# Optimization experiments

Hardware: AMD Instinct MI355X
Metric: run time of the kernel (lower is better)

The kernel has to match this reference:

```python
import jax, jax.numpy as jnp
import numpy as np

B, H, W, C = 32, 64, 64, 256


def setup_inputs() -> dict:
    key = jax.random.key(0)
    kq, kk, kv = jax.random.split(key, 3)
    query = jax.random.normal(kq, (B, H, W, C), dtype=jnp.float32)
    keys = jax.random.normal(kk, (B, H, W, C), dtype=jnp.float32)
    values = jax.random.normal(kv, (B, H, W, C), dtype=jnp.float32)
    return {"query": query, "keys": keys, "values": values}


def reference(query, keys, values):
    # A[b,q,k] = sum_{h,w} query[b,h,w,q] * keys[b,h,w,k]
    scores = jnp.einsum("bhwq,bhwk->bqk", query, keys)
    attn = jax.nn.softmax(scores, axis=-1)  # softmax over keys axis
    # out[b,q,h,w] = sum_k attn[b,q,k] * values[b,h,w,k]
    out = jnp.einsum("bqk,bhwk->bqhw", attn, values)
    return out
```

## Files before the change

kernel.cpp:

```cpp
#include <hip/hip_runtime.h>
#include <hip/hip_bf16.h>

#define B_  32
#define HW_ 4096
#define C_  256
#define S_LDS 40

using bf16x8 = __attribute__((ext_vector_type(8))) short;
using f32x4  = __attribute__((ext_vector_type(4))) float;
using u32x4  = __attribute__((ext_vector_type(4))) uint;

__device__ __forceinline__ ushort f2bf_rn(float x) {
    uint u = __builtin_bit_cast(uint, x);
    u += 0x7FFFu + ((u >> 16) & 1u);
    return (ushort)(u >> 16);
}
__device__ __forceinline__ uint pk_bf2(float a, float b) {
    return ((uint)f2bf_rn(b) << 16) | (uint)f2bf_rn(a);
}
__device__ __forceinline__ uint pk_rtz(float x0, float x1) {
    return __builtin_amdgcn_perm(__builtin_bit_cast(uint, x1),
                                 __builtin_bit_cast(uint, x0), 0x07060302u);
}
__device__ __forceinline__ void split2_rtz(float x0, float x1, uint& hi2, uint& lo2) {
    uint u0 = __builtin_bit_cast(uint, x0), u1 = __builtin_bit_cast(uint, x1);
    hi2 = __builtin_amdgcn_perm(u1, u0, 0x07060302u);
    float h0 = __builtin_bit_cast(float, u0 & 0xFFFF0000u);
    float h1 = __builtin_bit_cast(float, u1 & 0xFFFF0000u);
    lo2 = pk_rtz(x0 - h0, x1 - h1);
}

__global__ __launch_bounds__(256, 4) void scores_kernel(const float* __restrict__ qg,
                                                        const float* __restrict__ kg,
                                                        float* __restrict__ dst,
                                                        long slabStride) {
    int x  = blockIdx.x;
    int s  = x & 3;
    int tn = (x >> 2) & 3;
    int tm = (x >> 4) & 1;
    int b  = x >> 5;

    __shared__ __align__(16) ushort Qhi[128 * S_LDS], Qlo[128 * S_LDS];
    __shared__ __align__(16) ushort Khi[64 * S_LDS],  Klo[64 * S_LDS];

    int tid = threadIdx.x, lane = tid & 63, w = tid >> 6;
    int m0 = (w >> 1) * 64;
    int n0 = (w & 1) * 32;
    int g = lane >> 4, r16 = lane & 15;

    int cq = tid & 127;
    int hq = (tid >> 7) * 16;
    int ck = tid & 63;
    int hk = (tid >> 6) * 8;

    const float* qcol = qg + (size_t)b * HW_ * C_ + tm * 128 + cq;
    const float* kcol = kg + (size_t)b * HW_ * C_ + tn * 64 + ck;

    f32x4 acc[4][2];
#pragma unroll
    for (int i = 0; i < 4; ++i)
#pragma unroll
        for (int j = 0; j < 2; ++j) acc[i][j] = (f32x4){0.f, 0.f, 0.f, 0.f};

#define LOAD_QK(qr, kr, itv) {                                                 \
        int hw0 = s * 1024 + (itv) * 32;                                       \
        const float* qp = qcol + (size_t)(hw0 + hq) * C_;                      \
        _Pragma("unroll")                                                      \
        for (int j = 0; j < 16; ++j) qr[j] = qp[(size_t)j * C_];               \
        const float* kp = kcol + (size_t)(hw0 + hk) * C_;                      \
        _Pragma("unroll")                                                      \
        for (int j = 0; j < 8; ++j) kr[j] = kp[(size_t)j * C_];                \
    }

#define CONVERT_STORE(qr, kr) {                                                \
        uint qh[8], ql[8];                                                     \
        _Pragma("unroll")                                                      \
        for (int p = 0; p < 8; ++p) split2_rtz(qr[2*p], qr[2*p+1], qh[p], ql[p]); \
        int qb_ = cq * S_LDS + hq;                                             \
        *reinterpret_cast<u32x4*>(&Qhi[qb_])     = (u32x4){qh[0], qh[1], qh[2], qh[3]}; \
        *reinterpret_cast<u32x4*>(&Qhi[qb_ + 8]) = (u32x4){qh[4], qh[5], qh[6], qh[7]}; \
        *reinterpret_cast<u32x4*>(&Qlo[qb_])     = (u32x4){ql[0], ql[1], ql[2], ql[3]}; \
        *reinterpret_cast<u32x4*>(&Qlo[qb_ + 8]) = (u32x4){ql[4], ql[5], ql[6], ql[7]}; \
        uint kh[4], kl[4];                                                     \
        _Pragma("unroll")                                                      \
        for (int p = 0; p < 4; ++p) split2_rtz(kr[2*p], kr[2*p+1], kh[p], kl[p]); \
        int kb_ = ck * S_LDS + hk;                                             \
        *reinterpret_cast<u32x4*>(&Khi[kb_]) = (u32x4){kh[0], kh[1], kh[2], kh[3]}; \
        *reinterpret_cast<u32x4*>(&Klo[kb_]) = (u32x4){kl[0], kl[1], kl[2], kl[3]}; \
    }

#define MFMA_PHASE() {                                                         \
        __builtin_amdgcn_s_setprio(1);                                         \
        bf16x8 ahi[4], alo[4];                                                 \
        _Pragma("unroll")                                                      \
        for (int mi = 0; mi < 4; ++mi) {                                       \
            int off = (m0 + mi * 16 + r16) * S_LDS + g * 8;                    \
            ahi[mi] = *reinterpret_cast<const bf16x8*>(&Qhi[off]);             \
            alo[mi] = *reinterpret_cast<const bf16x8*>(&Qlo[off]);             \
        }                                                                      \
        _Pragma("unroll")                                                      \
        for (int ni = 0; ni < 2; ++ni) {                                       \
            int off = (n0 + ni * 16 + r16) * S_LDS + g * 8;                    \
            bf16x8 bhi = *reinterpret_cast<const bf16x8*>(&Khi[off]);          \
            bf16x8 blo = *reinterpret_cast<const bf16x8*>(&Klo[off]);          \
            _Pragma("unroll")                                                  \
            for (int mi = 0; mi < 4; ++mi) {                                   \
                acc[mi][ni] = __builtin_amdgcn_mfma_f32_16x16x32_bf16(ahi[mi], bhi, acc[mi][ni], 0, 0, 0); \
                acc[mi][ni] = __builtin_amdgcn_mfma_f32_16x16x32_bf16(ahi[mi], blo, acc[mi][ni], 0, 0, 0); \
                acc[mi][ni] = __builtin_amdgcn_mfma_f32_16x16x32_bf16(alo[mi], bhi, acc[mi][ni], 0, 0, 0); \
            }                                                                  \
        }                                                                      \
        __builtin_amdgcn_s_setprio(0);                                         \
    }

#define STEP(qc, kc, qn, kn, itv, doload) {                                    \
        if (doload) LOAD_QK(qn, kn, (itv) + 1);                                \
        __syncthreads();                                                       \
        CONVERT_STORE(qc, kc);                                                 \
        __syncthreads();                                                       \
        MFMA_PHASE();                                                          \
    }

    float qa[16], ka[8], qb[16], kb[8];
    LOAD_QK(qa, ka, 0);
    for (int p = 0; p < 16; ++p) {
        STEP(qa, ka, qb, kb, 2 * p, true);
        STEP(qb, kb, qa, ka, 2 * p + 1, p < 15);
    }

    float* base = dst + (size_t)s * slabStride;
#pragma unroll
    for (int mi = 0; mi < 4; ++mi)
#pragma unroll
        for (int ni = 0; ni < 2; ++ni)
#pragma unroll
            for (int r = 0; r < 4; ++r) {
                int qrow = tm * 128 + m0 + mi * 16 + g * 4 + r;
                int kc   = tn * 64 + n0 + ni * 16 + r16;
                float* p = base + ((size_t)b * 256 + qrow) * 256 + kc;
                if (slabStride) *p = acc[mi][ni][r];
                else            atomicAdd(p, acc[mi][ni][r]);
            }
#undef STEP
#undef MFMA_PHASE
#undef CONVERT_STORE
#undef LOAD_QK
}

__global__ __launch_bounds__(256) void softmax_kernel(const float* __restrict__ scores,
                                                      ushort* __restrict__ attn,
                                                      int nslab, long slabStride) {
    int wid  = blockIdx.x * 4 + (threadIdx.x >> 6);
    int lane = threadIdx.x & 63;
    const float* p0 = scores + (size_t)wid * 256 + lane * 4;
    float4 v = *reinterpret_cast<const float4*>(p0);
    for (int sl = 1; sl < nslab; ++sl) {
        const float4 t = *reinterpret_cast<const float4*>(p0 + (size_t)sl * slabStride);
        v.x += t.x; v.y += t.y; v.z += t.z; v.w += t.w;
    }
    float m = fmaxf(fmaxf(v.x, v.y), fmaxf(v.z, v.w));
#pragma unroll
    for (int off = 32; off; off >>= 1) m = fmaxf(m, __shfl_xor(m, off, 64));
    float e0 = __expf(v.x - m), e1 = __expf(v.y - m), e2 = __expf(v.z - m), e3 = __expf(v.w - m);
    float ssum = e0 + e1 + e2 + e3;
#pragma unroll
    for (int off = 32; off; off >>= 1) ssum += __shfl_xor(ssum, off, 64);
    float inv = 1.0f / ssum;
    uint2 o;
    o.x = pk_bf2(e0 * inv, e1 * inv);
    o.y = pk_bf2(e2 * inv, e3 * inv);
    *reinterpret_cast<uint2*>(attn + (size_t)wid * 256 + lane * 4) = o;
}

__global__ __launch_bounds__(256, 4) void pv_kernel(const ushort* __restrict__ attn,
                                                    const float* __restrict__ vg,
                                                    float* __restrict__ out) {
    int b   = blockIdx.x >> 6;
    int hw0 = (blockIdx.x & 63) * 64;
    int tid = threadIdx.x, lane = tid & 63, w = tid >> 6;
    int m0  = w * 64;
    int g   = lane >> 4, r16 = lane & 15;

    __shared__ __align__(16) float Vt[2 * 64 * 32];

    int srow = tid >> 2;
    int sslot = (tid & 3) * 2;
    int wi0 = srow * 32 + ((sslot ^ (srow & 7)) * 4);
    int wi1 = srow * 32 + (((sslot + 1) ^ (srow & 7)) * 4);
    const float* vstage = vg + ((size_t)(b * HW_ + hw0 + srow)) * C_ + sslot * 4;

    const ushort* abase = attn + (size_t)b * 256 * 256 + g * 8;

    f32x4 acc[4][4];
#pragma unroll
    for (int i = 0; i < 4; ++i)
#pragma unroll
        for (int j = 0; j < 4; ++j) acc[i][j] = (f32x4){0.f, 0.f, 0.f, 0.f};

    {
        f32x4 p0 = *reinterpret_cast<const f32x4*>(vstage);
        f32x4 p1 = *reinterpret_cast<const f32x4*>(vstage + 4);
        *reinterpret_cast<f32x4*>(&Vt[wi0]) = p0;
        *reinterpret_cast<f32x4*>(&Vt[wi1]) = p1;
    }
    __syncthreads();

    for (int p = 0; p < 8; ++p) {
        float* rbuf = &Vt[(p & 1) * 64 * 32];
        float* wbuf = &Vt[((p + 1) & 1) * 64 * 32];

        f32x4 n0v, n1v;
        if (p < 7) {
            n0v = *reinterpret_cast<const f32x4*>(vstage + (p + 1) * 32);
            n1v = *reinterpret_cast<const f32x4*>(vstage + (p + 1) * 32 + 4);
        }

        int k0 = p * 32;
        bf16x8 a[4];
#pragma unroll
        for (int mi = 0; mi < 4; ++mi)
            a[mi] = *reinterpret_cast<const bf16x8*>(abase + (size_t)(m0 + mi * 16 + r16) * 256 + k0);

#pragma unroll
        for (int ni = 0; ni < 4; ++ni) {
            int row = ni * 16 + r16, key = row & 7;
            f32x4 f0 = *reinterpret_cast<const f32x4*>(&rbuf[row * 32 + (((2 * g)     ^ key) * 4)]);
            f32x4 f1 = *reinterpret_cast<const f32x4*>(&rbuf[row * 32 + (((2 * g + 1) ^ key) * 4)]);
            bf16x8 bf = __builtin_bit_cast(bf16x8, (u32x4){
                pk_rtz(f0[0], f0[1]), pk_rtz(f0[2], f0[3]),
                pk_rtz(f1[0], f1[1]), pk_rtz(f1[2], f1[3])});
#pragma unroll
            for (int mi = 0; mi < 4; ++mi)
                acc[mi][ni] = __builtin_amdgcn_mfma_f32_16x16x32_bf16(a[mi], bf, acc[mi][ni], 0, 0, 0);
        }

        if (p < 7) {
            *reinterpret_cast<f32x4*>(&wbuf[wi0]) = n0v;
            *reinterpret_cast<f32x4*>(&wbuf[wi1]) = n1v;
            __syncthreads();
        }
    }

#pragma unroll
    for (int mi = 0; mi < 4; ++mi)
#pragma unroll
        for (int ni = 0; ni < 4; ++ni)
#pragma unroll
            for (int r = 0; r < 4; ++r) {
                int qrow = m0 + mi * 16 + g * 4 + r;
                int hw   = hw0 + ni * 16 + r16;
                out[((size_t)b * 256 + qrow) * 4096 + hw] = acc[mi][ni][r];
            }
}

extern "C" void kernel_launch(void* const* d_in, const int* in_sizes, int n_in,
                              void* d_out, int out_size, void* d_ws, size_t ws_size,
                              hipStream_t stream) {
    const float* q = (const float*)d_in[0];
    const float* k = (const float*)d_in[1];
    const float* v = (const float*)d_in[2];
    float* out = (float*)d_out;

    const size_t slab = (size_t)B_ * 256 * 256;
    const size_t needBytes = 4 * slab * 4 + slab * 2;
    float* scores = (float*)d_ws;

    if (ws_size >= needBytes) {
        ushort* attn = (ushort*)((char*)d_ws + 4 * slab * 4);
        scores_kernel<<<1024, 256, 0, stream>>>(q, k, scores, (long)slab);
        softmax_kernel<<<2048, 256, 0, stream>>>(scores, attn, 4, (long)slab);
        pv_kernel<<<2048, 256, 0, stream>>>(attn, v, out);
    } else {
        ushort* attn = (ushort*)((char*)d_ws + slab * 4);
        (void)hipMemsetAsync(d_ws, 0, slab * 4, stream);
        scores_kernel<<<1024, 256, 0, stream>>>(q, k, scores, 0L);
        softmax_kernel<<<2048, 256, 0, stream>>>(scores, attn, 1, 0L);
        pv_kernel<<<2048, 256, 0, stream>>>(attn, v, out);
    }
}
```

Baseline: 176.2 us.

## Load float2 pairs, triple-buffer global prefetch, and reorder block-index decomposition

The scores kernel now loads two adjacent channels per thread as float2 instead of scalar floats, which halves the number of load instructions. It also keeps three register buffers so global loads are issued two iterations ahead instead of one. The block index decomposition now puts tn and tm in the low bits so neighbouring blocks share the same HW slab, which may improve L2 locality. Occupancy hint is lowered from 4 to 3 blocks per CU to make room for the extra prefetch registers, at the cost of fewer resident waves.

After: 202.7 us. 15.1% more time.

```diff
diff --git a/kernel.cpp b/kernel.cpp
--- a/kernel.cpp
+++ b/kernel.cpp
@@ -30,14 +30,14 @@
     lo2 = pk_rtz(x0 - h0, x1 - h1);
 }
 
-__global__ __launch_bounds__(256, 4) void scores_kernel(const float* __restrict__ qg,
+__global__ __launch_bounds__(256, 3) void scores_kernel(const float* __restrict__ qg,
                                                         const float* __restrict__ kg,
                                                         float* __restrict__ dst,
                                                         long slabStride) {
     int x  = blockIdx.x;
-    int s  = x & 3;
-    int tn = (x >> 2) & 3;
-    int tm = (x >> 4) & 1;
+    int tn = x & 3;
+    int tm = (x >> 2) & 1;
+    int s  = (x >> 3) & 3;
     int b  = x >> 5;
 
     __shared__ __align__(16) ushort Qhi[128 * S_LDS], Qlo[128 * S_LDS];
@@ -48,13 +48,13 @@
     int n0 = (w & 1) * 32;
     int g = lane >> 4, r16 = lane & 15;
 
-    int cq = tid & 127;
-    int hq = (tid >> 7) * 16;
-    int ck = tid & 63;
-    int hk = (tid >> 6) * 8;
-
-    const float* qcol = qg + (size_t)b * HW_ * C_ + tm * 128 + cq;
-    const float* kcol = kg + (size_t)b * HW_ * C_ + tn * 64 + ck;
+    int qpair = tid & 63;
+    int hb    = (tid >> 6) * 8;
+    int kpair = tid & 31;
+    int hk    = (tid >> 5) * 4;
+
+    const float2* qbase2 = (const float2*)qg + (size_t)b * HW_ * 128 + tm * 64 + qpair;
+    const float2* kbase2 = (const float2*)kg + (size_t)b * HW_ * 128 + tn * 32 + kpair;
 
     f32x4 acc[4][2];
 #pragma unroll
@@ -62,31 +62,43 @@
 #pragma unroll
         for (int j = 0; j < 2; ++j) acc[i][j] = (f32x4){0.f, 0.f, 0.f, 0.f};
 
-#define LOAD_QK(qr, kr, itv) {                                                 \
+#define LOADQK(qr, kr, itv) {                                                  \
         int hw0 = s * 1024 + (itv) * 32;                                       \
-        const float* qp = qcol + (size_t)(hw0 + hq) * C_;                      \
-        _Pragma("unroll")                                                      \
-        for (int j = 0; j < 16; ++j) qr[j] = qp[(size_t)j * C_];               \
-        const float* kp = kcol + (size_t)(hw0 + hk) * C_;                      \
-        _Pragma("unroll")                                                      \
-        for (int j = 0; j < 8; ++j) kr[j] = kp[(size_t)j * C_];                \
+        const float2* qp = qbase2 + (size_t)(hw0 + hb) * 128;                  \
+        _Pragma("unroll")                                                      \
+        for (int j = 0; j < 8; ++j) qr[j] = qp[(size_t)j * 128];               \
+        const float2* kp = kbase2 + (size_t)(hw0 + hk) * 128;                  \
+        _Pragma("unroll")                                                      \
+        for (int j = 0; j < 4; ++j) kr[j] = kp[(size_t)j * 128];               \
     }
 
 #define CONVERT_STORE(qr, kr) {                                                \
-        uint qh[8], ql[8];                                                     \
-        _Pragma("unroll")                                                      \
-        for (int p = 0; p < 8; ++p) split2_rtz(qr[2*p], qr[2*p+1], qh[p], ql[p]); \
-        int qb_ = cq * S_LDS + hq;                                             \
-        *reinterpret_cast<u32x4*>(&Qhi[qb_])     = (u32x4){qh[0], qh[1], qh[2], qh[3]}; \
-        *reinterpret_cast<u32x4*>(&Qhi[qb_ + 8]) = (u32x4){qh[4], qh[5], qh[6], qh[7]}; \
-        *reinterpret_cast<u32x4*>(&Qlo[qb_])     = (u32x4){ql[0], ql[1], ql[2], ql[3]}; \
-        *reinterpret_cast<u32x4*>(&Qlo[qb_ + 8]) = (u32x4){ql[4], ql[5], ql[6], ql[7]}; \
-        uint kh[4], kl[4];                                                     \
-        _Pragma("unroll")                                                      \
-        for (int p = 0; p < 4; ++p) split2_rtz(kr[2*p], kr[2*p+1], kh[p], kl[p]); \
-        int kb_ = ck * S_LDS + hk;                                             \
-        *reinterpret_cast<u32x4*>(&Khi[kb_]) = (u32x4){kh[0], kh[1], kh[2], kh[3]}; \
-        *reinterpret_cast<u32x4*>(&Klo[kb_]) = (u32x4){kl[0], kl[1], kl[2], kl[3]}; \
+        uint h_[4], l_[4];                                                     \
+        split2_rtz(qr[0].x, qr[1].x, h_[0], l_[0]);                            \
+        split2_rtz(qr[2].x, qr[3].x, h_[1], l_[1]);                            \
+        split2_rtz(qr[4].x, qr[5].x, h_[2], l_[2]);                            \
+        split2_rtz(qr[6].x, qr[7].x, h_[3], l_[3]);                            \
+        int r0 = (2 * qpair) * S_LDS + hb;                                     \
+        *reinterpret_cast<u32x4*>(&Qhi[r0]) = (u32x4){h_[0], h_[1], h_[2], h_[3]}; \
+        *reinterpret_cast<u32x4*>(&Qlo[r0]) = (u32x4){l_[0], l_[1], l_[2], l_[3]}; \
+        split2_rtz(qr[0].y, qr[1].y, h_[0], l_[0]);                            \
+        split2_rtz(qr[2].y, qr[3].y, h_[1], l_[1]);                            \
+        split2_rtz(qr[4].y, qr[5].y, h_[2], l_[2]);                            \
+        split2_rtz(qr[6].y, qr[7].y, h_[3], l_[3]);                            \
+        int r1 = (2 * qpair + 1) * S_LDS + hb;                                 \
+        *reinterpret_cast<u32x4*>(&Qhi[r1]) = (u32x4){h_[0], h_[1], h_[2], h_[3]}; \
+        *reinterpret_cast<u32x4*>(&Qlo[r1]) = (u32x4){l_[0], l_[1], l_[2], l_[3]}; \
+        uint ha, hb2, la, lb;                                                  \
+        split2_rtz(kr[0].x, kr[1].x, ha, la);                                  \
+        split2_rtz(kr[2].x, kr[3].x, hb2, lb);                                 \
+        int rk0 = (2 * kpair) * S_LDS + hk;                                    \
+        *reinterpret_cast<uint2*>(&Khi[rk0]) = make_uint2(ha, hb2);            \
+        *reinterpret_cast<uint2*>(&Klo[rk0]) = make_uint2(la, lb);             \
+        split2_rtz(kr[0].y, kr[1].y, ha, la);                                  \
+        split2_rtz(kr[2].y, kr[3].y, hb2, lb);                                 \
+        int rk1 = (2 * kpair + 1) * S_LDS + hk;                                \
+        *reinterpret_cast<uint2*>(&Khi[rk1]) = make_uint2(ha, hb2);            \
+        *reinterpret_cast<uint2*>(&Klo[rk1]) = make_uint2(la, lb);             \
     }
 
 #define MFMA_PHASE() {                                                         \
@@ -114,19 +126,23 @@
     }
 
 #define STEP(qc, kc, qn, kn, itv, doload) {                                    \
-        if (doload) LOAD_QK(qn, kn, (itv) + 1);                                \
+        if (doload) LOADQK(qn, kn, (itv) + 2);                                 \
         __syncthreads();                                                       \
         CONVERT_STORE(qc, kc);                                                 \
         __syncthreads();                                                       \
         MFMA_PHASE();                                                          \
     }
 
-    float qa[16], ka[8], qb[16], kb[8];
-    LOAD_QK(qa, ka, 0);
-    for (int p = 0; p < 16; ++p) {
-        STEP(qa, ka, qb, kb, 2 * p, true);
-        STEP(qb, kb, qa, ka, 2 * p + 1, p < 15);
-    }
+    float2 qA[8], qB[8], qC[8], kA[4], kB[4], kC[4];
+    LOADQK(qA, kA, 0);
+    LOADQK(qB, kB, 1);
+    for (int p = 0; p < 10; ++p) {
+        STEP(qA, kA, qC, kC, 3 * p,     true);
+        STEP(qB, kB, qA, kA, 3 * p + 1, true);
+        STEP(qC, kC, qB, kB, 3 * p + 2, true);
+    }
+    STEP(qA, kA, qC, kC, 30, false);
+    STEP(qB, kB, qC, kC, 31, false);
 
     float* base = dst + (size_t)s * slabStride;
 #pragma unroll
@@ -144,7 +160,7 @@
 #undef STEP
 #undef MFMA_PHASE
 #undef CONVERT_STORE
-#undef LOAD_QK
+#undef LOADQK
 }
 
 __global__ __launch_bounds__(256) void softmax_kernel(const float* __restrict__ scores,
```

## Enlarge scores tile to 128x128 with 8-way split-K over HW

Applied to the files above, without the earlier changes.

The scores GEMM tile grows from 128x64 to 128x128 per block, so each loaded Q element is reused across twice as many key columns. This reduces redundant global reads of Q. To keep the same block count, split-K over the spatial axis doubles from 4 to 8 slabs, which doubles the partial-score workspace and the number of slabs the softmax kernel must sum. The larger accumulator raises register pressure, so the launch-bounds occupancy hint drops from 4 to 3 blocks.

Result: slower. 193.5 us (+9.8%).

```diff
diff --git a/kernel.cpp b/kernel.cpp
--- a/kernel.cpp
+++ b/kernel.cpp
@@ -30,63 +30,61 @@
     lo2 = pk_rtz(x0 - h0, x1 - h1);
 }
 
-__global__ __launch_bounds__(256, 4) void scores_kernel(const float* __restrict__ qg,
+__global__ __launch_bounds__(256, 3) void scores_kernel(const float* __restrict__ qg,
                                                         const float* __restrict__ kg,
                                                         float* __restrict__ dst,
                                                         long slabStride) {
     int x  = blockIdx.x;
-    int s  = x & 3;
-    int tn = (x >> 2) & 3;
+    int s  = x & 7;
+    int tn = (x >> 3) & 1;
     int tm = (x >> 4) & 1;
     int b  = x >> 5;
 
     __shared__ __align__(16) ushort Qhi[128 * S_LDS], Qlo[128 * S_LDS];
-    __shared__ __align__(16) ushort Khi[64 * S_LDS],  Klo[64 * S_LDS];
+    __shared__ __align__(16) ushort Khi[128 * S_LDS], Klo[128 * S_LDS];
 
     int tid = threadIdx.x, lane = tid & 63, w = tid >> 6;
     int m0 = (w >> 1) * 64;
-    int n0 = (w & 1) * 32;
+    int n0 = (w & 1) * 64;
     int g = lane >> 4, r16 = lane & 15;
 
-    int cq = tid & 127;
-    int hq = (tid >> 7) * 16;
-    int ck = tid & 63;
-    int hk = (tid >> 6) * 8;
-
-    const float* qcol = qg + (size_t)b * HW_ * C_ + tm * 128 + cq;
-    const float* kcol = kg + (size_t)b * HW_ * C_ + tn * 64 + ck;
-
-    f32x4 acc[4][2];
+    int cc = tid & 127;
+    int hh = (tid >> 7) * 16;
+
+    const float* qcol = qg + (size_t)b * HW_ * C_ + tm * 128 + cc;
+    const float* kcol = kg + (size_t)b * HW_ * C_ + tn * 128 + cc;
+
+    f32x4 acc[4][4];
 #pragma unroll
     for (int i = 0; i < 4; ++i)
 #pragma unroll
-        for (int j = 0; j < 2; ++j) acc[i][j] = (f32x4){0.f, 0.f, 0.f, 0.f};
+        for (int j = 0; j < 4; ++j) acc[i][j] = (f32x4){0.f, 0.f, 0.f, 0.f};
 
 #define LOAD_QK(qr, kr, itv) {                                                 \
-        int hw0 = s * 1024 + (itv) * 32;                                       \
-        const float* qp = qcol + (size_t)(hw0 + hq) * C_;                      \
+        int hw0 = s * 512 + (itv) * 32 + hh;                                   \
+        const float* qp = qcol + (size_t)hw0 * C_;                             \
+        const float* kp = kcol + (size_t)hw0 * C_;                             \
         _Pragma("unroll")                                                      \
         for (int j = 0; j < 16; ++j) qr[j] = qp[(size_t)j * C_];               \
-        const float* kp = kcol + (size_t)(hw0 + hk) * C_;                      \
-        _Pragma("unroll")                                                      \
-        for (int j = 0; j < 8; ++j) kr[j] = kp[(size_t)j * C_];                \
+        _Pragma("unroll")                                                      \
+        for (int j = 0; j < 16; ++j) kr[j] = kp[(size_t)j * C_];               \
     }
 
 #define CONVERT_STORE(qr, kr) {                                                \
-        uint qh[8], ql[8];                                                     \
-        _Pragma("unroll")                                                      \
-        for (int p = 0; p < 8; ++p) split2_rtz(qr[2*p], qr[2*p+1], qh[p], ql[p]); \
-        int qb_ = cq * S_LDS + hq;                                             \
-        *reinterpret_cast<u32x4*>(&Qhi[qb_])     = (u32x4){qh[0], qh[1], qh[2], qh[3]}; \
-        *reinterpret_cast<u32x4*>(&Qhi[qb_ + 8]) = (u32x4){qh[4], qh[5], qh[6], qh[7]}; \
-        *reinterpret_cast<u32x4*>(&Qlo[qb_])     = (u32x4){ql[0], ql[1], ql[2], ql[3]}; \
-        *reinterpret_cast<u32x4*>(&Qlo[qb_ + 8]) = (u32x4){ql[4], ql[5], ql[6], ql[7]}; \
-        uint kh[4], kl[4];                                                     \
-        _Pragma("unroll")                                                      \
-        for (int p = 0; p < 4; ++p) split2_rtz(kr[2*p], kr[2*p+1], kh[p], kl[p]); \
-        int kb_ = ck * S_LDS + hk;                                             \
-        *reinterpret_cast<u32x4*>(&Khi[kb_]) = (u32x4){kh[0], kh[1], kh[2], kh[3]}; \
-        *reinterpret_cast<u32x4*>(&Klo[kb_]) = (u32x4){kl[0], kl[1], kl[2], kl[3]}; \
+        uint h_[8], l_[8];                                                     \
+        _Pragma("unroll")                                                      \
+        for (int p = 0; p < 8; ++p) split2_rtz(qr[2*p], qr[2*p+1], h_[p], l_[p]); \
+        int b_ = cc * S_LDS + hh;                                              \
+        *reinterpret_cast<u32x4*>(&Qhi[b_])     = (u32x4){h_[0], h_[1], h_[2], h_[3]}; \
+        *reinterpret_cast<u32x4*>(&Qhi[b_ + 8]) = (u32x4){h_[4], h_[5], h_[6], h_[7]}; \
+        *reinterpret_cast<u32x4*>(&Qlo[b_])     = (u32x4){l_[0], l_[1], l_[2], l_[3]}; \
+        *reinterpret_cast<u32x4*>(&Qlo[b_ + 8]) = (u32x4){l_[4], l_[5], l_[6], l_[7]}; \
+        _Pragma("unroll")                                                      \
+        for (int p = 0; p < 8; ++p) split2_rtz(kr[2*p], kr[2*p+1], h_[p], l_[p]); \
+        *reinterpret_cast<u32x4*>(&Khi[b_])     = (u32x4){h_[0], h_[1], h_[2], h_[3]}; \
+        *reinterpret_cast<u32x4*>(&Khi[b_ + 8]) = (u32x4){h_[4], h_[5], h_[6], h_[7]}; \
+        *reinterpret_cast<u32x4*>(&Klo[b_])     = (u32x4){l_[0], l_[1], l_[2], l_[3]}; \
+        *reinterpret_cast<u32x4*>(&Klo[b_ + 8]) = (u32x4){l_[4], l_[5], l_[6], l_[7]}; \
     }
 
 #define MFMA_PHASE() {                                                         \
@@ -99,7 +97,7 @@
             alo[mi] = *reinterpret_cast<const bf16x8*>(&Qlo[off]);             \
         }                                                                      \
         _Pragma("unroll")                                                      \
-        for (int ni = 0; ni < 2; ++ni) {                                       \
+        for (int ni = 0; ni < 4; ++ni) {                                       \
             int off = (n0 + ni * 16 + r16) * S_LDS + g * 8;                    \
             bf16x8 bhi = *reinterpret_cast<const bf16x8*>(&Khi[off]);          \
             bf16x8 blo = *reinterpret_cast<const bf16x8*>(&Klo[off]);          \
@@ -121,23 +119,23 @@
         MFMA_PHASE();                                                          \
     }
 
-    float qa[16], ka[8], qb[16], kb[8];
+    float qa[16], ka[16], qb[16], kb[16];
     LOAD_QK(qa, ka, 0);
-    for (int p = 0; p < 16; ++p) {
+    for (int p = 0; p < 8; ++p) {
         STEP(qa, ka, qb, kb, 2 * p, true);
-        STEP(qb, kb, qa, ka, 2 * p + 1, p < 15);
+        STEP(qb, kb, qa, ka, 2 * p + 1, p < 7);
     }
 
     float* base = dst + (size_t)s * slabStride;
 #pragma unroll
     for (int mi = 0; mi < 4; ++mi)
 #pragma unroll
-        for (int ni = 0; ni < 2; ++ni)
+        for (int ni = 0; ni < 4; ++ni)
 #pragma unroll
             for (int r = 0; r < 4; ++r) {
                 int qrow = tm * 128 + m0 + mi * 16 + g * 4 + r;
-                int kc   = tn * 64 + n0 + ni * 16 + r16;
-                float* p = base + ((size_t)b * 256 + qrow) * 256 + kc;
+                int kc2  = tn * 128 + n0 + ni * 16 + r16;
+                float* p = base + ((size_t)b * 256 + qrow) * 256 + kc2;
                 if (slabStride) *p = acc[mi][ni][r];
                 else            atomicAdd(p, acc[mi][ni][r]);
             }
@@ -262,13 +260,13 @@
     float* out = (float*)d_out;
 
     const size_t slab = (size_t)B_ * 256 * 256;
-    const size_t needBytes = 4 * slab * 4 + slab * 2;
+    const size_t needBytes = 8 * slab * 4 + slab * 2;
     float* scores = (float*)d_ws;
 
     if (ws_size >= needBytes) {
-        ushort* attn = (ushort*)((char*)d_ws + 4 * slab * 4);
+        ushort* attn = (ushort*)((char*)d_ws + 8 * slab * 4);
         scores_kernel<<<1024, 256, 0, stream>>>(q, k, scores, (long)slab);
-        softmax_kernel<<<2048, 256, 0, stream>>>(scores, attn, 4, (long)slab);
+        softmax_kernel<<<2048, 256, 0, stream>>>(scores, attn, 8, (long)slab);
         pv_kernel<<<2048, 256, 0, stream>>>(attn, v, out);
     } else {
         ushort* attn = (ushort*)((char*)d_ws + slab * 4);
```
